# Kernel tuning notes

Measured on AMD Instinct MI355X. Metric: run time of the kernel, lower is better.

The kernel has to match this reference:

```python
import jax, jax.numpy as jnp
import numpy as np

B, T, D = 16, 1024, 512      # batch, query time, model hidden
C = 4096                     # context entries
DC = 512                     # context hidden
A = 512                      # attndim
P = 512                      # proj hidden


def setup_inputs() -> dict:
    key = jax.random.key(0)
    ks = jax.random.split(key, 10)
    s = lambda fan_in: 1.0 / np.sqrt(fan_in)
    return {
        "model_embed": jax.random.normal(ks[0], (B, T, D), jnp.float32),
        "context_embed": jax.random.normal(ks[1], (C, DC), jnp.float32),
        "Wq": jax.random.uniform(ks[2], (D, A), jnp.float32, -s(D), s(D)),
        "bq": jax.random.uniform(ks[3], (A,), jnp.float32, -s(D), s(D)),
        "Wk": jax.random.uniform(ks[4], (DC, A), jnp.float32, -s(DC), s(DC)),
        "bk": jax.random.uniform(ks[5], (A,), jnp.float32, -s(DC), s(DC)),
        "Wv": jax.random.uniform(ks[6], (DC, A), jnp.float32, -s(DC), s(DC)),
        "bv": jax.random.uniform(ks[7], (A,), jnp.float32, -s(DC), s(DC)),
        "Wo": jax.random.uniform(ks[8], (A, P), jnp.float32, -s(A), s(A)),
        "bo": jax.random.uniform(ks[9], (P,), jnp.float32, -s(A), s(A)),
    }


def reference(model_embed, context_embed, Wq, bq, Wk, bk, Wv, bv, Wo, bo):
    q = model_embed @ Wq + bq            # [B, T, A]
    k = context_embed @ Wk + bk          # [C, A]
    v = context_embed @ Wv + bv          # [C, A]
    scale = 1.0 / jnp.sqrt(jnp.asarray(q.shape[-1], q.dtype))
    scores = jnp.einsum('ck,btk->btc', k, q) * scale   # [B, T, C]
    attn = jax.nn.softmax(scores, axis=-1)             # softmax over context
    x = jnp.einsum('ck,btc->btk', v, attn)             # [B, T, A]
    return x @ Wo + bo                                 # [B, T, P]
```

## Files before the change

### kernel.cpp

```cpp
#include <hip/hip_runtime.h>

#define MB_T 16384
#define DD   512
#define CC   4096
#define AA   512
#define PP   512

typedef __attribute__((ext_vector_type(4))) float f32x4;
typedef __attribute__((ext_vector_type(8))) short short8;

#define MFMA16(a, b, c) __builtin_amdgcn_mfma_f32_16x16x32_bf16((a), (b), (c), 0, 0, 0)

__device__ __forceinline__ unsigned short f2bf(float f) {
  union { float f; unsigned int u; } cv; cv.f = f;
  unsigned int u = cv.u;
  return (unsigned short)((u + 0x7FFFu + ((u >> 16) & 1u)) >> 16);
}
__device__ __forceinline__ float bf2f(unsigned short u) {
  union { unsigned int i; float f; } c; c.i = (unsigned int)u << 16; return c.f;
}

__device__ __forceinline__ void gload16(const unsigned short* g, unsigned short* l) {
  __builtin_amdgcn_global_load_lds(
      (const __attribute__((address_space(1))) unsigned int*)g,
      (__attribute__((address_space(3))) unsigned int*)l, 16, 0, 0);
}

__global__ void cast_bf16_kernel(const float* __restrict__ in,
                                 unsigned short* __restrict__ out, int n4) {
  int i = blockIdx.x * blockDim.x + threadIdx.x;
  int stride = gridDim.x * blockDim.x;
  for (; i < n4; i += stride) {
    float4 v = reinterpret_cast<const float4*>(in)[i];
    ushort4 o;
    o.x = f2bf(v.x); o.y = f2bf(v.y); o.z = f2bf(v.z); o.w = f2bf(v.w);
    reinterpret_cast<ushort4*>(out)[i] = o;
  }
}

__global__ __launch_bounds__(256) void transpose_cast_kernel(
    const float* __restrict__ W, unsigned short* __restrict__ WT, int rows, int cols) {
  __shared__ float t_s[32][33];
  int bi = blockIdx.y * 32, bj = blockIdx.x * 32;
  int r = threadIdx.x >> 3, c4 = (threadIdx.x & 7) * 4;
  float4 v = *reinterpret_cast<const float4*>(W + (size_t)(bi + r) * cols + bj + c4);
  t_s[r][c4 + 0] = v.x; t_s[r][c4 + 1] = v.y;
  t_s[r][c4 + 2] = v.z; t_s[r][c4 + 3] = v.w;
  __syncthreads();
  ushort4 o;
  o.x = f2bf(t_s[c4 + 0][r]);
  o.y = f2bf(t_s[c4 + 1][r]);
  o.z = f2bf(t_s[c4 + 2][r]);
  o.w = f2bf(t_s[c4 + 3][r]);
  *reinterpret_cast<ushort4*>(WT + (size_t)(bj + r) * rows + bi + c4) = o;
}

__global__ __launch_bounds__(256) void rowdot_kernel(
    const unsigned short* __restrict__ k, const float* __restrict__ bq,
    float* __restrict__ outv, float scale) {
  const int lane = threadIdx.x & 63, wid = threadIdx.x >> 6;
  const int row = blockIdx.x * 4 + wid;
  const unsigned short* kr = k + (size_t)row * AA + lane * 8;
  float s = 0.f;
  ushort4 a = *reinterpret_cast<const ushort4*>(kr);
  ushort4 b = *reinterpret_cast<const ushort4*>(kr + 4);
  const float* bqp = bq + lane * 8;
  s += bf2f(a.x) * bqp[0]; s += bf2f(a.y) * bqp[1];
  s += bf2f(a.z) * bqp[2]; s += bf2f(a.w) * bqp[3];
  s += bf2f(b.x) * bqp[4]; s += bf2f(b.y) * bqp[5];
  s += bf2f(b.z) * bqp[6]; s += bf2f(b.w) * bqp[7];
#pragma unroll
  for (int d = 1; d < 64; d <<= 1) s += __shfl_xor(s, d);
  if (lane == 0) outv[row] = s * scale;
}

template <int MODE>
__global__ __launch_bounds__(256) void gemm2p_kernel(
    const unsigned short* __restrict__ A, const unsigned short* __restrict__ BT,
    const float* __restrict__ bias, const float* __restrict__ colbias,
    const float* __restrict__ rowsum_in, float* __restrict__ rowsum_out,
    void* __restrict__ Cout, int M, int N, int K, float alpha) {
  __shared__ unsigned short a_s[2][4096];
  __shared__ unsigned short b_s[2][4096];
  const int tid = threadIdx.x;
  const int lane = tid & 63, wid = tid >> 6;
  const int hq = lane >> 4, lq = lane & 15;
  const int wm = wid >> 1, wn = wid & 1;

  const int gx = gridDim.x;
  const int nwg = gx * gridDim.y;
  const int orig = blockIdx.y * gx + blockIdx.x;
  const int swz = (orig & 7) * (nwg >> 3) + (orig >> 3);
  const int bx = swz % gx, by = swz / gx;
  const int brow = by * 128, bcol = bx * 128;

  const unsigned short* ap = A + (size_t)(brow + (tid >> 2)) * K + (tid & 3) * 8;
  const unsigned short* bp = BT + (size_t)(bcol + (tid >> 2)) * K + (tid & 3) * 8;
  const size_t rstep = (size_t)64 * K;
  const int ldsoff = wid * 512;

  const int nt = K >> 5;
  gload16(ap, a_s[0] + ldsoff);
  gload16(ap + rstep, a_s[0] + ldsoff + 2048);
  gload16(bp, b_s[0] + ldsoff);
  gload16(bp + rstep, b_s[0] + ldsoff + 2048);
  __syncthreads();

  f32x4 acc[4][4] = {};
  for (int t = 0; t < nt; ++t) {
    const int cur = t & 1;
    if (t + 1 < nt) {
      const int k0 = (t + 1) * 32;
      gload16(ap + k0, a_s[cur ^ 1] + ldsoff);
      gload16(ap + rstep + k0, a_s[cur ^ 1] + ldsoff + 2048);
      gload16(bp + k0, b_s[cur ^ 1] + ldsoff);
      gload16(bp + rstep + k0, b_s[cur ^ 1] + ldsoff + 2048);
    }
    short8 af[4], bfv[4];
#pragma unroll
    for (int mf = 0; mf < 4; ++mf)
      af[mf] = *reinterpret_cast<const short8*>(&a_s[cur][(wm * 64 + mf * 16 + lq) * 32 + hq * 8]);
#pragma unroll
    for (int nf = 0; nf < 4; ++nf)
      bfv[nf] = *reinterpret_cast<const short8*>(&b_s[cur][(wn * 64 + nf * 16 + lq) * 32 + hq * 8]);
#pragma unroll
    for (int mf = 0; mf < 4; ++mf)
#pragma unroll
      for (int nf = 0; nf < 4; ++nf)
        acc[mf][nf] = MFMA16(af[mf], bfv[nf], acc[mf][nf]);
    if (t + 1 < nt) __syncthreads();
  }

  if (MODE == 3) {
    float cb[4];
#pragma unroll
    for (int nf = 0; nf < 4; ++nf) cb[nf] = colbias[bcol + wn * 64 + nf * 16 + lq];
#pragma unroll
    for (int mf = 0; mf < 4; ++mf)
#pragma unroll
      for (int i = 0; i < 4; ++i) {
        const int rowg = brow + wm * 64 + mf * 16 + hq * 4 + i;
        float s = 0.f;
#pragma unroll
        for (int nf = 0; nf < 4; ++nf) {
          float p = __expf(acc[mf][nf][i] + cb[nf]);
          s += p;
          ((unsigned short*)Cout)[(size_t)rowg * N + bcol + wn * 64 + nf * 16 + lq] = f2bf(p);
        }
        s += __shfl_xor(s, 1);
        s += __shfl_xor(s, 2);
        s += __shfl_xor(s, 4);
        s += __shfl_xor(s, 8);
        if (lq == 0) atomicAdd(rowsum_out + rowg, s);
      }
  } else if (MODE == 5) {
#pragma unroll
    for (int mf = 0; mf < 4; ++mf)
#pragma unroll
      for (int i = 0; i < 4; ++i) {
        const int rowg = brow + wm * 64 + mf * 16 + hq * 4 + i;
        const float inv = 1.0f / rowsum_in[rowg];
#pragma unroll
        for (int nf = 0; nf < 4; ++nf) {
          const int colg = bcol + wn * 64 + nf * 16 + lq;
          ((float*)Cout)[(size_t)rowg * N + colg] = acc[mf][nf][i] * inv + bias[colg];
        }
      }
  } else {
#pragma unroll
    for (int nf = 0; nf < 4; ++nf) {
      const int colg = bcol + wn * 64 + nf * 16 + lq;
      const float bv = bias ? bias[colg] : 0.f;
#pragma unroll
      for (int mf = 0; mf < 4; ++mf) {
        const int rowg0 = brow + wm * 64 + mf * 16 + hq * 4;
#pragma unroll
        for (int i = 0; i < 4; ++i)
          ((unsigned short*)Cout)[(size_t)(rowg0 + i) * N + colg] =
              f2bf((acc[mf][nf][i] + bv) * alpha);
      }
    }
  }
}

extern "C" void kernel_launch(void* const* d_in, const int* in_sizes, int n_in,
                              void* d_out, int out_size, void* d_ws, size_t ws_size,
                              hipStream_t stream) {
  const float* model = (const float*)d_in[0];
  const float* ctx   = (const float*)d_in[1];
  const float* Wq = (const float*)d_in[2]; const float* bq = (const float*)d_in[3];
  const float* Wk = (const float*)d_in[4]; const float* bk = (const float*)d_in[5];
  const float* Wv = (const float*)d_in[6]; const float* bv = (const float*)d_in[7];
  const float* Wo = (const float*)d_in[8]; const float* bo = (const float*)d_in[9];
  float* out = (float*)d_out;

  char* ws = (char*)d_ws;
  size_t off = 0;
  auto alloc = [&](size_t bytes) -> void* {
    void* p = ws + off;
    off += (bytes + 255) & ~(size_t)255;
    return p;
  };
  unsigned short* model_bf = (unsigned short*)alloc((size_t)MB_T * DD * 2);
  unsigned short* ctx_bf   = (unsigned short*)alloc((size_t)CC * DD * 2);
  unsigned short* k_bf     = (unsigned short*)alloc((size_t)CC * AA * 2);
  unsigned short* v_bf     = (unsigned short*)alloc((size_t)CC * AA * 2);
  unsigned short* Wq_bf    = (unsigned short*)alloc((size_t)DD * AA * 2);
  unsigned short* WkT = (unsigned short*)alloc((size_t)DD * AA * 2);
  unsigned short* WvT = (unsigned short*)alloc((size_t)DD * AA * 2);
  unsigned short* WoT = (unsigned short*)alloc((size_t)AA * PP * 2);
  unsigned short* KqT_bf = (unsigned short*)alloc((size_t)CC * DD * 2);
  unsigned short* W2T_bf = (unsigned short*)alloc((size_t)PP * CC * 2);
  float* bqk  = (float*)alloc((size_t)CC * 4);
  float* lsum = (float*)alloc((size_t)MB_T * 4);
  unsigned short* P_bf = (unsigned short*)alloc((size_t)MB_T * CC * 2);

  const float scale = 0.04419417382415922f;

  cast_bf16_kernel<<<2048, 256, 0, stream>>>(model, model_bf, MB_T * DD / 4);
  cast_bf16_kernel<<<1024, 256, 0, stream>>>(ctx, ctx_bf, CC * DD / 4);
  cast_bf16_kernel<<<256, 256, 0, stream>>>(Wq, Wq_bf, DD * AA / 4);

  dim3 tg(16, 16);
  transpose_cast_kernel<<<tg, 256, 0, stream>>>(Wk, WkT, DD, AA);
  transpose_cast_kernel<<<tg, 256, 0, stream>>>(Wv, WvT, DD, AA);
  transpose_cast_kernel<<<tg, 256, 0, stream>>>(Wo, WoT, AA, PP);

  gemm2p_kernel<0><<<dim3(AA / 128, CC / 128), 256, 0, stream>>>(
      ctx_bf, WkT, bk, nullptr, nullptr, nullptr, k_bf, CC, AA, DD, 1.0f);
  gemm2p_kernel<0><<<dim3(AA / 128, CC / 128), 256, 0, stream>>>(
      ctx_bf, WvT, bv, nullptr, nullptr, nullptr, v_bf, CC, AA, DD, 1.0f);

  gemm2p_kernel<0><<<dim3(DD / 128, CC / 128), 256, 0, stream>>>(
      k_bf, Wq_bf, nullptr, nullptr, nullptr, nullptr, KqT_bf, CC, DD, AA, scale);
  rowdot_kernel<<<CC / 4, 256, 0, stream>>>(k_bf, bq, bqk, scale);

  gemm2p_kernel<0><<<dim3(CC / 128, PP / 128), 256, 0, stream>>>(
      WoT, v_bf, nullptr, nullptr, nullptr, nullptr, W2T_bf, PP, CC, AA, 1.0f);

  hipMemsetAsync(lsum, 0, (size_t)MB_T * 4, stream);
  gemm2p_kernel<3><<<dim3(CC / 128, MB_T / 128), 256, 0, stream>>>(
      model_bf, KqT_bf, nullptr, bqk, nullptr, lsum, P_bf, MB_T, CC, DD, 1.0f);

  gemm2p_kernel<5><<<dim3(PP / 128, MB_T / 128), 256, 0, stream>>>(
      P_bf, W2T_bf, bo, nullptr, lsum, nullptr, out, MB_T, PP, CC, 1.0f);
}
```

Baseline: 417.5 us.

## Precompose weight products and add swizzled double-buffered GEMM for attention core

The ctx projection chain is reassociated so that Wq·Wk^T and Wo^T·Wv^T are formed first as small 512x512 products. The per-context K·Wq and V·Wo terms then come from ctx times these fused weights, replacing separate K/V projections. The two large GEMMs (scores with exp, and P·W2) move to a new kernel with 64-wide K tiles, XOR-swizzled LDS, two-stage prefetch and setprio around MFMA. This cuts several intermediate GEMMs and transposes and aims to speed the dominant GEMMs, at the cost of extra bf16 rounding on the composed weights.

Result: no change. 410.5 us (-1.7%).

```diff
diff --git a/kernel.cpp b/kernel.cpp
--- a/kernel.cpp
+++ b/kernel.cpp
@@ -56,15 +56,15 @@
 }
 
 __global__ __launch_bounds__(256) void rowdot_kernel(
-    const unsigned short* __restrict__ k, const float* __restrict__ bq,
+    const unsigned short* __restrict__ mat, const float* __restrict__ vec,
     float* __restrict__ outv, float scale) {
   const int lane = threadIdx.x & 63, wid = threadIdx.x >> 6;
   const int row = blockIdx.x * 4 + wid;
-  const unsigned short* kr = k + (size_t)row * AA + lane * 8;
+  const unsigned short* kr = mat + (size_t)row * 512 + lane * 8;
   float s = 0.f;
   ushort4 a = *reinterpret_cast<const ushort4*>(kr);
   ushort4 b = *reinterpret_cast<const ushort4*>(kr + 4);
-  const float* bqp = bq + lane * 8;
+  const float* bqp = vec + lane * 8;
   s += bf2f(a.x) * bqp[0]; s += bf2f(a.y) * bqp[1];
   s += bf2f(a.z) * bqp[2]; s += bf2f(a.w) * bqp[3];
   s += bf2f(b.x) * bqp[4]; s += bf2f(b.y) * bqp[5];
@@ -77,9 +77,8 @@
 template <int MODE>
 __global__ __launch_bounds__(256) void gemm2p_kernel(
     const unsigned short* __restrict__ A, const unsigned short* __restrict__ BT,
-    const float* __restrict__ bias, const float* __restrict__ colbias,
-    const float* __restrict__ rowsum_in, float* __restrict__ rowsum_out,
-    void* __restrict__ Cout, int M, int N, int K, float alpha) {
+    const float* __restrict__ bias, void* __restrict__ Cout,
+    int M, int N, int K, float alpha) {
   __shared__ unsigned short a_s[2][4096];
   __shared__ unsigned short b_s[2][4096];
   const int tid = threadIdx.x;
@@ -129,6 +128,141 @@
       for (int nf = 0; nf < 4; ++nf)
         acc[mf][nf] = MFMA16(af[mf], bfv[nf], acc[mf][nf]);
     if (t + 1 < nt) __syncthreads();
+  }
+
+  if (MODE == 1) {
+#pragma unroll
+    for (int nf = 0; nf < 4; ++nf) {
+      const int colg = bcol + wn * 64 + nf * 16 + lq;
+      const float bv = bias ? bias[colg] : 0.f;
+#pragma unroll
+      for (int mf = 0; mf < 4; ++mf) {
+        const int rowg0 = brow + wm * 64 + mf * 16 + hq * 4;
+        ushort4 pk;
+        pk.x = f2bf(acc[mf][nf][0] + bv);
+        pk.y = f2bf(acc[mf][nf][1] + bv);
+        pk.z = f2bf(acc[mf][nf][2] + bv);
+        pk.w = f2bf(acc[mf][nf][3] + bv);
+        *reinterpret_cast<ushort4*>((unsigned short*)Cout + (size_t)colg * M + rowg0) = pk;
+      }
+    }
+  } else {
+#pragma unroll
+    for (int nf = 0; nf < 4; ++nf) {
+      const int colg = bcol + wn * 64 + nf * 16 + lq;
+      const float bv = bias ? bias[colg] : 0.f;
+#pragma unroll
+      for (int mf = 0; mf < 4; ++mf) {
+        const int rowg0 = brow + wm * 64 + mf * 16 + hq * 4;
+#pragma unroll
+        for (int i = 0; i < 4; ++i)
+          ((unsigned short*)Cout)[(size_t)(rowg0 + i) * N + colg] =
+              f2bf((acc[mf][nf][i] + bv) * alpha);
+      }
+    }
+  }
+}
+
+template <int MODE>
+__global__ __launch_bounds__(256, 2) void gemm_dp_kernel(
+    const unsigned short* __restrict__ A, const unsigned short* __restrict__ BT,
+    const float* __restrict__ bias, const float* __restrict__ colbias,
+    const float* __restrict__ rowsum_in, float* __restrict__ rowsum_out,
+    void* __restrict__ Cout, int M, int N, int K) {
+  __shared__ unsigned short a_s[2][8192];
+  __shared__ unsigned short b_s[2][8192];
+  const int tid = threadIdx.x;
+  const int lane = tid & 63, wid = tid >> 6;
+  const int hq = lane >> 4, lq = lane & 15;
+  const int wm = wid >> 1, wn = wid & 1;
+
+  const int gx = gridDim.x;
+  const int nwg = gx * gridDim.y;
+  const int orig = blockIdx.y * gx + blockIdx.x;
+  const int swz = (orig & 7) * (nwg >> 3) + (orig >> 3);
+  const int bx = swz % gx, by = swz / gx;
+  const int brow = by * 128, bcol = bx * 128;
+
+  const int srow = tid >> 3;
+  const int schunk = (tid & 7) ^ (srow & 7);
+  const unsigned short* agp = A + (size_t)(brow + srow) * K + schunk * 8;
+  const unsigned short* bgp = BT + (size_t)(bcol + srow) * K + schunk * 8;
+  const size_t row32 = (size_t)32 * K;
+  const int ldst = wid * 512;
+
+  const int nt = K >> 6;
+#pragma unroll
+  for (int j = 0; j < 4; ++j) {
+    gload16(agp + j * row32, &a_s[0][j * 2048 + ldst]);
+    gload16(bgp + j * row32, &b_s[0][j * 2048 + ldst]);
+  }
+#pragma unroll
+  for (int j = 0; j < 4; ++j) {
+    gload16(agp + j * row32 + 64, &a_s[1][j * 2048 + ldst]);
+    gload16(bgp + j * row32 + 64, &b_s[1][j * 2048 + ldst]);
+  }
+  asm volatile("s_waitcnt vmcnt(8)" ::: "memory");
+  __builtin_amdgcn_s_barrier();
+
+  const int aoff = (wm * 64 + lq) * 64;
+  const int boff = (wn * 64 + lq) * 64;
+  const int cx0 = ((hq) ^ (lq & 7)) * 8;
+  const int cx1 = ((4 + hq) ^ (lq & 7)) * 8;
+
+  f32x4 acc[4][4] = {};
+  for (int t = 0; t < nt; ++t) {
+    const int cur = t & 1;
+    const unsigned short* as0 = a_s[cur];
+    const unsigned short* bs0 = b_s[cur];
+    short8 ar[2][2], br[4][2];
+#pragma unroll
+    for (int f = 0; f < 2; ++f) {
+      ar[f][0] = *reinterpret_cast<const short8*>(as0 + aoff + f * 1024 + cx0);
+      ar[f][1] = *reinterpret_cast<const short8*>(as0 + aoff + f * 1024 + cx1);
+    }
+#pragma unroll
+    for (int f = 0; f < 4; ++f) {
+      br[f][0] = *reinterpret_cast<const short8*>(bs0 + boff + f * 1024 + cx0);
+      br[f][1] = *reinterpret_cast<const short8*>(bs0 + boff + f * 1024 + cx1);
+    }
+    __builtin_amdgcn_s_setprio(1);
+#pragma unroll
+    for (int f = 0; f < 2; ++f)
+#pragma unroll
+      for (int n = 0; n < 4; ++n) {
+        acc[f][n] = MFMA16(ar[f][0], br[n][0], acc[f][n]);
+        acc[f][n] = MFMA16(ar[f][1], br[n][1], acc[f][n]);
+      }
+    __builtin_amdgcn_s_setprio(0);
+    __builtin_amdgcn_s_barrier();
+#pragma unroll
+    for (int f = 0; f < 2; ++f) {
+      ar[f][0] = *reinterpret_cast<const short8*>(as0 + aoff + (f + 2) * 1024 + cx0);
+      ar[f][1] = *reinterpret_cast<const short8*>(as0 + aoff + (f + 2) * 1024 + cx1);
+    }
+    __builtin_amdgcn_s_setprio(1);
+#pragma unroll
+    for (int f = 0; f < 2; ++f)
+#pragma unroll
+      for (int n = 0; n < 4; ++n) {
+        acc[f + 2][n] = MFMA16(ar[f][0], br[n][0], acc[f + 2][n]);
+        acc[f + 2][n] = MFMA16(ar[f][1], br[n][1], acc[f + 2][n]);
+      }
+    __builtin_amdgcn_s_setprio(0);
+    __builtin_amdgcn_s_barrier();
+    if (t + 2 < nt) {
+      const size_t k0 = (size_t)(t + 2) * 64;
+#pragma unroll
+      for (int j = 0; j < 4; ++j) {
+        gload16(agp + j * row32 + k0, &a_s[cur][j * 2048 + ldst]);
+        gload16(bgp + j * row32 + k0, &b_s[cur][j * 2048 + ldst]);
+      }
+      asm volatile("s_waitcnt vmcnt(8)" ::: "memory");
+      __builtin_amdgcn_s_barrier();
+    } else if (t + 1 < nt) {
+      asm volatile("s_waitcnt vmcnt(0)" ::: "memory");
+      __builtin_amdgcn_s_barrier();
+    }
   }
 
   if (MODE == 3) {
@@ -153,7 +287,7 @@
         s += __shfl_xor(s, 8);
         if (lq == 0) atomicAdd(rowsum_out + rowg, s);
       }
-  } else if (MODE == 5) {
+  } else {
 #pragma unroll
     for (int mf = 0; mf < 4; ++mf)
 #pragma unroll
@@ -166,20 +300,6 @@
           ((float*)Cout)[(size_t)rowg * N + colg] = acc[mf][nf][i] * inv + bias[colg];
         }
       }
-  } else {
-#pragma unroll
-    for (int nf = 0; nf < 4; ++nf) {
-      const int colg = bcol + wn * 64 + nf * 16 + lq;
-      const float bv = bias ? bias[colg] : 0.f;
-#pragma unroll
-      for (int mf = 0; mf < 4; ++mf) {
-        const int rowg0 = brow + wm * 64 + mf * 16 + hq * 4;
-#pragma unroll
-        for (int i = 0; i < 4; ++i)
-          ((unsigned short*)Cout)[(size_t)(rowg0 + i) * N + colg] =
-              f2bf((acc[mf][nf][i] + bv) * alpha);
-      }
-    }
   }
 }
 
@@ -203,14 +323,17 @@
   };
   unsigned short* model_bf = (unsigned short*)alloc((size_t)MB_T * DD * 2);
   unsigned short* ctx_bf   = (unsigned short*)alloc((size_t)CC * DD * 2);
-  unsigned short* k_bf     = (unsigned short*)alloc((size_t)CC * AA * 2);
-  unsigned short* v_bf     = (unsigned short*)alloc((size_t)CC * AA * 2);
-  unsigned short* Wq_bf    = (unsigned short*)alloc((size_t)DD * AA * 2);
-  unsigned short* WkT = (unsigned short*)alloc((size_t)DD * AA * 2);
-  unsigned short* WvT = (unsigned short*)alloc((size_t)DD * AA * 2);
-  unsigned short* WoT = (unsigned short*)alloc((size_t)AA * PP * 2);
-  unsigned short* KqT_bf = (unsigned short*)alloc((size_t)CC * DD * 2);
-  unsigned short* W2T_bf = (unsigned short*)alloc((size_t)PP * CC * 2);
+  unsigned short* Wq_bf = (unsigned short*)alloc((size_t)DD * AA * 2);
+  unsigned short* Wk_bf = (unsigned short*)alloc((size_t)DD * AA * 2);
+  unsigned short* Wv_bf = (unsigned short*)alloc((size_t)DD * AA * 2);
+  unsigned short* WoT   = (unsigned short*)alloc((size_t)AA * PP * 2);
+  unsigned short* WkqT_bf = (unsigned short*)alloc((size_t)DD * DD * 2);
+  unsigned short* WvoT_bf = (unsigned short*)alloc((size_t)PP * DD * 2);
+  unsigned short* KqT_bf  = (unsigned short*)alloc((size_t)CC * DD * 2);
+  unsigned short* W2T_bf  = (unsigned short*)alloc((size_t)PP * CC * 2);
+  float* bkq  = (float*)alloc((size_t)DD * 4);
+  float* bvo  = (float*)alloc((size_t)PP * 4);
+  float* wkbq = (float*)alloc((size_t)DD * 4);
   float* bqk  = (float*)alloc((size_t)CC * 4);
   float* lsum = (float*)alloc((size_t)MB_T * 4);
   unsigned short* P_bf = (unsigned short*)alloc((size_t)MB_T * CC * 2);
@@ -220,28 +343,29 @@
   cast_bf16_kernel<<<2048, 256, 0, stream>>>(model, model_bf, MB_T * DD / 4);
   cast_bf16_kernel<<<1024, 256, 0, stream>>>(ctx, ctx_bf, CC * DD / 4);
   cast_bf16_kernel<<<256, 256, 0, stream>>>(Wq, Wq_bf, DD * AA / 4);
-
-  dim3 tg(16, 16);
-  transpose_cast_kernel<<<tg, 256, 0, stream>>>(Wk, WkT, DD, AA);
-  transpose_cast_kernel<<<tg, 256, 0, stream>>>(Wv, WvT, DD, AA);
-  transpose_cast_kernel<<<tg, 256, 0, stream>>>(Wo, WoT, AA, PP);
-
-  gemm2p_kernel<0><<<dim3(AA / 128, CC / 128), 256, 0, stream>>>(
-      ctx_bf, WkT, bk, nullptr, nullptr, nullptr, k_bf, CC, AA, DD, 1.0f);
-  gemm2p_kernel<0><<<dim3(AA / 128, CC / 128), 256, 0, stream>>>(
-      ctx_bf, WvT, bv, nullptr, nullptr, nullptr, v_bf, CC, AA, DD, 1.0f);
-
-  gemm2p_kernel<0><<<dim3(DD / 128, CC / 128), 256, 0, stream>>>(
-      k_bf, Wq_bf, nullptr, nullptr, nullptr, nullptr, KqT_bf, CC, DD, AA, scale);
-  rowdot_kernel<<<CC / 4, 256, 0, stream>>>(k_bf, bq, bqk, scale);
-
-  gemm2p_kernel<0><<<dim3(CC / 128, PP / 128), 256, 0, stream>>>(
-      WoT, v_bf, nullptr, nullptr, nullptr, nullptr, W2T_bf, PP, CC, AA, 1.0f);
+  cast_bf16_kernel<<<256, 256, 0, stream>>>(Wk, Wk_bf, DD * AA / 4);
+  cast_bf16_kernel<<<256, 256, 0, stream>>>(Wv, Wv_bf, DD * AA / 4);
+  transpose_cast_kernel<<<dim3(16, 16), 256, 0, stream>>>(Wo, WoT, AA, PP);
+
+  rowdot_kernel<<<DD / 4, 256, 0, stream>>>(Wq_bf, bk, bkq, scale);
+  rowdot_kernel<<<DD / 4, 256, 0, stream>>>(Wk_bf, bq, wkbq, scale);
+  rowdot_kernel<<<PP / 4, 256, 0, stream>>>(WoT, bv, bvo, 1.0f);
+  rowdot_kernel<<<CC / 4, 256, 0, stream>>>(ctx_bf, wkbq, bqk, 1.0f);
+
+  gemm2p_kernel<0><<<dim3(4, 4), 256, 0, stream>>>(
+      Wq_bf, Wk_bf, nullptr, WkqT_bf, DD, DD, AA, scale);
+  gemm2p_kernel<0><<<dim3(4, 4), 256, 0, stream>>>(
+      WoT, Wv_bf, nullptr, WvoT_bf, PP, DD, AA, 1.0f);
+
+  gemm2p_kernel<0><<<dim3(4, 32), 256, 0, stream>>>(
+      ctx_bf, WkqT_bf, bkq, KqT_bf, CC, DD, DD, 1.0f);
+  gemm2p_kernel<1><<<dim3(4, 32), 256, 0, stream>>>(
+      ctx_bf, WvoT_bf, bvo, W2T_bf, CC, PP, DD, 1.0f);
 
   hipMemsetAsync(lsum, 0, (size_t)MB_T * 4, stream);
-  gemm2p_kernel<3><<<dim3(CC / 128, MB_T / 128), 256, 0, stream>>>(
-      model_bf, KqT_bf, nullptr, bqk, nullptr, lsum, P_bf, MB_T, CC, DD, 1.0f);
-
-  gemm2p_kernel<5><<<dim3(PP / 128, MB_T / 128), 256, 0, stream>>>(
-      P_bf, W2T_bf, bo, nullptr, lsum, nullptr, out, MB_T, PP, CC, 1.0f);
-}
+  gemm_dp_kernel<3><<<dim3(32, 128), 256, 0, stream>>>(
+      model_bf, KqT_bf, nullptr, bqk, nullptr, lsum, P_bf, MB_T, CC, DD);
+
+  gemm_dp_kernel<5><<<dim3(4, 128), 256, 0, stream>>>(
+      P_bf, W2T_bf, bo, nullptr, lsum, nullptr, out, MB_T, PP, CC);
+}
```

## Fold weight products, stage softmax tile via LDS, replace atomics with partial sums

Applied to the files above, without the earlier changes.

Precomputes Wq·Wk^T and Wo·Wv^T weight products so the context-side GEMMs run directly on ctx with folded biases, writing W2T transposed via a new epilogue mode. The exp/score GEMM now stages its bf16 tile in LDS for coalesced 16-byte stores, and writes per-block row partial sums instead of atomics, reduced by a new kernel. The final GEMM uses a 64-row tile to raise block count, and launch bounds request 4 waves per SIMD. This trades extra small launches and rounding from folded products for less atomic traffic and better stores.

Result: faster. 363.1 us (-13.0%).

```diff
diff --git a/kernel.cpp b/kernel.cpp
--- a/kernel.cpp
+++ b/kernel.cpp
@@ -56,15 +56,15 @@
 }
 
 __global__ __launch_bounds__(256) void rowdot_kernel(
-    const unsigned short* __restrict__ k, const float* __restrict__ bq,
+    const unsigned short* __restrict__ mat, const float* __restrict__ vec,
     float* __restrict__ outv, float scale) {
   const int lane = threadIdx.x & 63, wid = threadIdx.x >> 6;
   const int row = blockIdx.x * 4 + wid;
-  const unsigned short* kr = k + (size_t)row * AA + lane * 8;
+  const unsigned short* kr = mat + (size_t)row * 512 + lane * 8;
   float s = 0.f;
   ushort4 a = *reinterpret_cast<const ushort4*>(kr);
   ushort4 b = *reinterpret_cast<const ushort4*>(kr + 4);
-  const float* bqp = bq + lane * 8;
+  const float* bqp = vec + lane * 8;
   s += bf2f(a.x) * bqp[0]; s += bf2f(a.y) * bqp[1];
   s += bf2f(a.z) * bqp[2]; s += bf2f(a.w) * bqp[3];
   s += bf2f(b.x) * bqp[4]; s += bf2f(b.y) * bqp[5];
@@ -74,14 +74,30 @@
   if (lane == 0) outv[row] = s * scale;
 }
 
-template <int MODE>
-__global__ __launch_bounds__(256) void gemm2p_kernel(
+__global__ __launch_bounds__(256) void reduce_lsum_kernel(
+    const float* __restrict__ lsp, float* __restrict__ lsum) {
+  int m = blockIdx.x * blockDim.x + threadIdx.x;
+  const float4* p = reinterpret_cast<const float4*>(lsp + (size_t)m * 64);
+  float s = 0.f;
+#pragma unroll
+  for (int j = 0; j < 16; ++j) { float4 v = p[j]; s += v.x + v.y + v.z + v.w; }
+  lsum[m] = s;
+}
+
+template <int MODE, int TM>
+__global__ __launch_bounds__(256, 4) void gemm2p_kernel(
     const unsigned short* __restrict__ A, const unsigned short* __restrict__ BT,
     const float* __restrict__ bias, const float* __restrict__ colbias,
-    const float* __restrict__ rowsum_in, float* __restrict__ rowsum_out,
+    const float* __restrict__ rowsum_in, float* __restrict__ psum_out,
     void* __restrict__ Cout, int M, int N, int K, float alpha) {
-  __shared__ unsigned short a_s[2][4096];
-  __shared__ unsigned short b_s[2][4096];
+  constexpr int MFR = TM / 32;
+  constexpr int WROW = TM / 2;
+  constexpr int ASZ = TM * 32;
+  constexpr int BSZ = 128 * 32;
+  constexpr int STG = 2 * ASZ + 2 * BSZ;
+  constexpr int TOT = (MODE == 3 && STG < 128 * 136) ? 128 * 136 : STG;
+  __shared__ unsigned short lds[TOT];
+
   const int tid = threadIdx.x;
   const int lane = tid & 63, wid = tid >> 6;
   const int hq = lane >> 4, lq = lane & 15;
@@ -92,39 +108,44 @@
   const int orig = blockIdx.y * gx + blockIdx.x;
   const int swz = (orig & 7) * (nwg >> 3) + (orig >> 3);
   const int bx = swz % gx, by = swz / gx;
-  const int brow = by * 128, bcol = bx * 128;
+  const int brow = by * TM, bcol = bx * 128;
 
   const unsigned short* ap = A + (size_t)(brow + (tid >> 2)) * K + (tid & 3) * 8;
   const unsigned short* bp = BT + (size_t)(bcol + (tid >> 2)) * K + (tid & 3) * 8;
-  const size_t rstep = (size_t)64 * K;
-  const int ldsoff = wid * 512;
+  const size_t row64 = (size_t)64 * K;
 
   const int nt = K >> 5;
-  gload16(ap, a_s[0] + ldsoff);
-  gload16(ap + rstep, a_s[0] + ldsoff + 2048);
-  gload16(bp, b_s[0] + ldsoff);
-  gload16(bp + rstep, b_s[0] + ldsoff + 2048);
+#pragma unroll
+  for (int j = 0; j < TM / 64; ++j)
+    gload16(ap + j * row64, lds + wid * 512 + j * 2048);
+  gload16(bp, lds + 2 * ASZ + wid * 512);
+  gload16(bp + row64, lds + 2 * ASZ + wid * 512 + 2048);
   __syncthreads();
 
-  f32x4 acc[4][4] = {};
+  f32x4 acc[MFR][4] = {};
   for (int t = 0; t < nt; ++t) {
     const int cur = t & 1;
     if (t + 1 < nt) {
       const int k0 = (t + 1) * 32;
-      gload16(ap + k0, a_s[cur ^ 1] + ldsoff);
-      gload16(ap + rstep + k0, a_s[cur ^ 1] + ldsoff + 2048);
-      gload16(bp + k0, b_s[cur ^ 1] + ldsoff);
-      gload16(bp + rstep + k0, b_s[cur ^ 1] + ldsoff + 2048);
-    }
-    short8 af[4], bfv[4];
-#pragma unroll
-    for (int mf = 0; mf < 4; ++mf)
-      af[mf] = *reinterpret_cast<const short8*>(&a_s[cur][(wm * 64 + mf * 16 + lq) * 32 + hq * 8]);
+      unsigned short* an = lds + (cur ^ 1) * ASZ + wid * 512;
+      unsigned short* bn = lds + 2 * ASZ + (cur ^ 1) * BSZ + wid * 512;
+#pragma unroll
+      for (int j = 0; j < TM / 64; ++j)
+        gload16(ap + k0 + j * row64, an + j * 2048);
+      gload16(bp + k0, bn);
+      gload16(bp + k0 + row64, bn + 2048);
+    }
+    const unsigned short* as0 = lds + cur * ASZ;
+    const unsigned short* bs0 = lds + 2 * ASZ + cur * BSZ;
+    short8 af[MFR], bfv[4];
+#pragma unroll
+    for (int mf = 0; mf < MFR; ++mf)
+      af[mf] = *reinterpret_cast<const short8*>(&as0[(wm * WROW + mf * 16 + lq) * 32 + hq * 8]);
 #pragma unroll
     for (int nf = 0; nf < 4; ++nf)
-      bfv[nf] = *reinterpret_cast<const short8*>(&b_s[cur][(wn * 64 + nf * 16 + lq) * 32 + hq * 8]);
-#pragma unroll
-    for (int mf = 0; mf < 4; ++mf)
+      bfv[nf] = *reinterpret_cast<const short8*>(&bs0[(wn * 64 + nf * 16 + lq) * 32 + hq * 8]);
+#pragma unroll
+    for (int mf = 0; mf < MFR; ++mf)
 #pragma unroll
       for (int nf = 0; nf < 4; ++nf)
         acc[mf][nf] = MFMA16(af[mf], bfv[nf], acc[mf][nf]);
@@ -135,30 +156,39 @@
     float cb[4];
 #pragma unroll
     for (int nf = 0; nf < 4; ++nf) cb[nf] = colbias[bcol + wn * 64 + nf * 16 + lq];
-#pragma unroll
-    for (int mf = 0; mf < 4; ++mf)
+    __syncthreads();
+#pragma unroll
+    for (int mf = 0; mf < MFR; ++mf)
 #pragma unroll
       for (int i = 0; i < 4; ++i) {
-        const int rowg = brow + wm * 64 + mf * 16 + hq * 4 + i;
+        const int rowl = wm * WROW + mf * 16 + hq * 4 + i;
         float s = 0.f;
 #pragma unroll
         for (int nf = 0; nf < 4; ++nf) {
           float p = __expf(acc[mf][nf][i] + cb[nf]);
           s += p;
-          ((unsigned short*)Cout)[(size_t)rowg * N + bcol + wn * 64 + nf * 16 + lq] = f2bf(p);
+          lds[rowl * 136 + wn * 64 + nf * 16 + lq] = f2bf(p);
         }
         s += __shfl_xor(s, 1);
         s += __shfl_xor(s, 2);
         s += __shfl_xor(s, 4);
         s += __shfl_xor(s, 8);
-        if (lq == 0) atomicAdd(rowsum_out + rowg, s);
-      }
+        if (lq == 0) psum_out[(size_t)(brow + rowl) * 64 + bx * 2 + wn] = s;
+      }
+    __syncthreads();
+#pragma unroll
+    for (int j = 0; j < 8; ++j) {
+      const int chunk = j * 256 + tid;
+      const int row = chunk >> 4, c = chunk & 15;
+      short8 v = *reinterpret_cast<const short8*>(&lds[row * 136 + c * 8]);
+      *reinterpret_cast<short8*>((unsigned short*)Cout + (size_t)(brow + row) * N + bcol + c * 8) = v;
+    }
   } else if (MODE == 5) {
 #pragma unroll
-    for (int mf = 0; mf < 4; ++mf)
+    for (int mf = 0; mf < MFR; ++mf)
 #pragma unroll
       for (int i = 0; i < 4; ++i) {
-        const int rowg = brow + wm * 64 + mf * 16 + hq * 4 + i;
+        const int rowg = brow + wm * WROW + mf * 16 + hq * 4 + i;
         const float inv = 1.0f / rowsum_in[rowg];
 #pragma unroll
         for (int nf = 0; nf < 4; ++nf) {
@@ -166,14 +196,30 @@
           ((float*)Cout)[(size_t)rowg * N + colg] = acc[mf][nf][i] * inv + bias[colg];
         }
       }
-  } else {
+  } else if (MODE == 1) {
 #pragma unroll
     for (int nf = 0; nf < 4; ++nf) {
       const int colg = bcol + wn * 64 + nf * 16 + lq;
       const float bv = bias ? bias[colg] : 0.f;
 #pragma unroll
-      for (int mf = 0; mf < 4; ++mf) {
-        const int rowg0 = brow + wm * 64 + mf * 16 + hq * 4;
+      for (int mf = 0; mf < MFR; ++mf) {
+        const int rowg0 = brow + wm * WROW + mf * 16 + hq * 4;
+        ushort4 pk;
+        pk.x = f2bf(acc[mf][nf][0] + bv);
+        pk.y = f2bf(acc[mf][nf][1] + bv);
+        pk.z = f2bf(acc[mf][nf][2] + bv);
+        pk.w = f2bf(acc[mf][nf][3] + bv);
+        *reinterpret_cast<ushort4*>((unsigned short*)Cout + (size_t)colg * M + rowg0) = pk;
+      }
+    }
+  } else {
+#pragma unroll
+    for (int nf = 0; nf < 4; ++nf) {
+      const int colg = bcol + wn * 64 + nf * 16 + lq;
+      const float bv = bias ? bias[colg] : 0.f;
+#pragma unroll
+      for (int mf = 0; mf < MFR; ++mf) {
+        const int rowg0 = brow + wm * WROW + mf * 16 + hq * 4;
 #pragma unroll
         for (int i = 0; i < 4; ++i)
           ((unsigned short*)Cout)[(size_t)(rowg0 + i) * N + colg] =
@@ -203,15 +249,19 @@
   };
   unsigned short* model_bf = (unsigned short*)alloc((size_t)MB_T * DD * 2);
   unsigned short* ctx_bf   = (unsigned short*)alloc((size_t)CC * DD * 2);
-  unsigned short* k_bf     = (unsigned short*)alloc((size_t)CC * AA * 2);
-  unsigned short* v_bf     = (unsigned short*)alloc((size_t)CC * AA * 2);
-  unsigned short* Wq_bf    = (unsigned short*)alloc((size_t)DD * AA * 2);
-  unsigned short* WkT = (unsigned short*)alloc((size_t)DD * AA * 2);
-  unsigned short* WvT = (unsigned short*)alloc((size_t)DD * AA * 2);
-  unsigned short* WoT = (unsigned short*)alloc((size_t)AA * PP * 2);
-  unsigned short* KqT_bf = (unsigned short*)alloc((size_t)CC * DD * 2);
-  unsigned short* W2T_bf = (unsigned short*)alloc((size_t)PP * CC * 2);
+  unsigned short* Wq_bf = (unsigned short*)alloc((size_t)DD * AA * 2);
+  unsigned short* Wk_bf = (unsigned short*)alloc((size_t)DD * AA * 2);
+  unsigned short* Wv_bf = (unsigned short*)alloc((size_t)DD * AA * 2);
+  unsigned short* WoT   = (unsigned short*)alloc((size_t)AA * PP * 2);
+  unsigned short* WkqT_bf = (unsigned short*)alloc((size_t)DD * DD * 2);
+  unsigned short* WvoT_bf = (unsigned short*)alloc((size_t)PP * DD * 2);
+  unsigned short* KqT_bf  = (unsigned short*)alloc((size_t)CC * DD * 2);
+  unsigned short* W2T_bf  = (unsigned short*)alloc((size_t)PP * CC * 2);
+  float* bkq  = (float*)alloc((size_t)DD * 4);
+  float* bvo  = (float*)alloc((size_t)PP * 4);
+  float* wkbq = (float*)alloc((size_t)DD * 4);
   float* bqk  = (float*)alloc((size_t)CC * 4);
+  float* lsp  = (float*)alloc((size_t)MB_T * 64 * 4);
   float* lsum = (float*)alloc((size_t)MB_T * 4);
   unsigned short* P_bf = (unsigned short*)alloc((size_t)MB_T * CC * 2);
 
@@ -220,28 +270,30 @@
   cast_bf16_kernel<<<2048, 256, 0, stream>>>(model, model_bf, MB_T * DD / 4);
   cast_bf16_kernel<<<1024, 256, 0, stream>>>(ctx, ctx_bf, CC * DD / 4);
   cast_bf16_kernel<<<256, 256, 0, stream>>>(Wq, Wq_bf, DD * AA / 4);
-
-  dim3 tg(16, 16);
-  transpose_cast_kernel<<<tg, 256, 0, stream>>>(Wk, WkT, DD, AA);
-  transpose_cast_kernel<<<tg, 256, 0, stream>>>(Wv, WvT, DD, AA);
-  transpose_cast_kernel<<<tg, 256, 0, stream>>>(Wo, WoT, AA, PP);
-
-  gemm2p_kernel<0><<<dim3(AA / 128, CC / 128), 256, 0, stream>>>(
-      ctx_bf, WkT, bk, nullptr, nullptr, nullptr, k_bf, CC, AA, DD, 1.0f);
-  gemm2p_kernel<0><<<dim3(AA / 128, CC / 128), 256, 0, stream>>>(
-      ctx_bf, WvT, bv, nullptr, nullptr, nullptr, v_bf, CC, AA, DD, 1.0f);
-
-  gemm2p_kernel<0><<<dim3(DD / 128, CC / 128), 256, 0, stream>>>(
-      k_bf, Wq_bf, nullptr, nullptr, nullptr, nullptr, KqT_bf, CC, DD, AA, scale);
-  rowdot_kernel<<<CC / 4, 256, 0, stream>>>(k_bf, bq, bqk, scale);
-
-  gemm2p_kernel<0><<<dim3(CC / 128, PP / 128), 256, 0, stream>>>(
-      WoT, v_bf, nullptr, nullptr, nullptr, nullptr, W2T_bf, PP, CC, AA, 1.0f);
-
-  hipMemsetAsync(lsum, 0, (size_t)MB_T * 4, stream);
-  gemm2p_kernel<3><<<dim3(CC / 128, MB_T / 128), 256, 0, stream>>>(
-      model_bf, KqT_bf, nullptr, bqk, nullptr, lsum, P_bf, MB_T, CC, DD, 1.0f);
-
-  gemm2p_kernel<5><<<dim3(PP / 128, MB_T / 128), 256, 0, stream>>>(
+  cast_bf16_kernel<<<256, 256, 0, stream>>>(Wk, Wk_bf, DD * AA / 4);
+  cast_bf16_kernel<<<256, 256, 0, stream>>>(Wv, Wv_bf, DD * AA / 4);
+  transpose_cast_kernel<<<dim3(16, 16), 256, 0, stream>>>(Wo, WoT, AA, PP);
+
+  rowdot_kernel<<<DD / 4, 256, 0, stream>>>(Wq_bf, bk, bkq, scale);
+  rowdot_kernel<<<DD / 4, 256, 0, stream>>>(Wk_bf, bq, wkbq, scale);
+  rowdot_kernel<<<PP / 4, 256, 0, stream>>>(WoT, bv, bvo, 1.0f);
+  rowdot_kernel<<<CC / 4, 256, 0, stream>>>(ctx_bf, wkbq, bqk, 1.0f);
+
+  gemm2p_kernel<0, 128><<<dim3(4, 4), 256, 0, stream>>>(
+      Wq_bf, Wk_bf, nullptr, nullptr, nullptr, nullptr, WkqT_bf, DD, DD, AA, scale);
+  gemm2p_kernel<0, 128><<<dim3(4, 4), 256, 0, stream>>>(
+      WoT, Wv_bf, nullptr, nullptr, nullptr, nullptr, WvoT_bf, PP, DD, AA, 1.0f);
+
+  gemm2p_kernel<0, 128><<<dim3(4, 32), 256, 0, stream>>>(
+      ctx_bf, WkqT_bf, bkq, nullptr, nullptr, nullptr, KqT_bf, CC, DD, DD, 1.0f);
+  gemm2p_kernel<1, 128><<<dim3(4, 32), 256, 0, stream>>>(
+      ctx_bf, WvoT_bf, bvo, nullptr, nullptr, nullptr, W2T_bf, CC, PP, DD, 1.0f);
+
+  gemm2p_kernel<3, 128><<<dim3(32, 128), 256, 0, stream>>>(
+      model_bf, KqT_bf, nullptr, bqk, nullptr, lsp, P_bf, MB_T, CC, DD, 1.0f);
+
+  reduce_lsum_kernel<<<MB_T / 256, 256, 0, stream>>>(lsp, lsum);
+
+  gemm2p_kernel<5, 64><<<dim3(4, 256), 256, 0, stream>>>(
       P_bf, W2T_bf, bo, nullptr, lsum, nullptr, out, MB_T, PP, CC, 1.0f);
 }
```
